# Kernel tuning notes

Hardware: AMD Instinct MI355X
Metric: run time of the kernel (lower is better)

The kernel has to match this reference:

```python
import jax, jax.numpy as jnp
import numpy as np

N_NODES = 100000
N_EDGES = 1600000
N_GRAPHS = 128
VOCAB = 10000
EMBED = 32
HID = 64
CLASSES = 2


def setup_inputs() -> dict:
    key = jax.random.key(0)
    ks = jax.random.split(key, 10)
    node_ids = jax.random.randint(ks[0], (N_NODES,), 0, VOCAB)
    edge_index = jax.random.randint(ks[1], (2, N_EDGES), 0, N_NODES)
    batch = jnp.sort(jax.random.randint(ks[2], (N_NODES,), 0, N_GRAPHS))
    s_e = 1.0 / np.sqrt(EMBED)
    s_h = 1.0 / np.sqrt(HID)
    return {
        "node_ids": node_ids,
        "edge_index": edge_index,
        "batch": batch,
        "embed_table": jax.random.normal(ks[3], (VOCAB, EMBED), jnp.float32),
        "W1_l": jax.random.normal(ks[4], (HID, EMBED), jnp.float32) * s_e,
        "W1_r": jax.random.normal(ks[5], (HID, EMBED), jnp.float32) * s_e,
        "b1": jnp.zeros((HID,), jnp.float32),
        "W2_l": jax.random.normal(ks[6], (HID, HID), jnp.float32) * s_h,
        "W2_r": jax.random.normal(ks[7], (HID, HID), jnp.float32) * s_h,
        "b2": jnp.zeros((HID,), jnp.float32),
        "W_lin": jax.random.normal(ks[8], (CLASSES, HID), jnp.float32) * s_h,
        "b_lin": jnp.zeros((CLASSES,), jnp.float32),
    }


def _sage_conv(x, src, dst, W_l, W_r, b):
    # mean-aggregate neighbor features: messages flow src -> dst
    msg_sum = jax.ops.segment_sum(x[src], dst, num_segments=x.shape[0])
    cnt = jax.ops.segment_sum(jnp.ones((src.shape[0], 1), x.dtype), dst,
                              num_segments=x.shape[0])
    mean = msg_sum / jnp.maximum(cnt, 1.0)
    return mean @ W_l.T + x @ W_r.T + b


def _global_mean_pool(x, batch, num_graphs):
    s = jax.ops.segment_sum(x, batch, num_segments=num_graphs)
    cnt = jax.ops.segment_sum(jnp.ones((x.shape[0], 1), x.dtype), batch,
                              num_segments=num_graphs)
    return s / jnp.maximum(cnt, 1.0)


def reference(node_ids, edge_index, batch, embed_table,
              W1_l, W1_r, b1, W2_l, W2_r, b2, W_lin, b_lin):
    src, dst = edge_index[0], edge_index[1]
    x = embed_table[node_ids]                       # [N, EMBED]
    x = jax.nn.relu(_sage_conv(x, src, dst, W1_l, W1_r, b1))  # [N, HID]
    x = jax.nn.relu(_sage_conv(x, src, dst, W2_l, W2_r, b2))  # [N, HID]
    g = _global_mean_pool(x, batch, N_GRAPHS)       # [G, HID]
    return g @ W_lin.T + b_lin                      # [G, CLASSES]
```

## Files before the change

### kernel.cpp

```cpp
#include <hip/hip_runtime.h>
#include <hip/hip_fp16.h>
#include <hip/hip_fp8.h>

#define N_NODES 100000
#define N_EDGES 1600000
#define N_GRAPHS 128
#define EMBED 32
#define HID 64
#define NBUCK 1563
#define CAP 1280
#define CHUNK 128
#define NGRP (N_EDGES / CHUNK)
#define PTILE 8192
#define NTILE ((N_EDGES + PTILE - 1) / PTILE)
#define TP 200
#define NPGRP 2048
#define PPER ((N_NODES + NPGRP - 1) / NPGRP)

typedef _Float16 f16x8 __attribute__((ext_vector_type(8)));
typedef float f32x4 __attribute__((ext_vector_type(4)));
typedef float f32x2 __attribute__((ext_vector_type(2)));
typedef unsigned short u16x8 __attribute__((ext_vector_type(8)));

__device__ __forceinline__ float fp8_to_f(unsigned char b) {
    __hip_fp8_e4m3 t; t.__x = (__hip_fp8_storage_t)b; return (float)t;
}
__device__ __forceinline__ unsigned char f_to_fp8(float f) {
    __hip_fp8_e4m3 t(f); return (unsigned char)t.__x;
}
__device__ __forceinline__ unsigned short h_bits(float f) {
    __half h = __float2half(f); return *(unsigned short*)&h;
}

#if defined(__has_builtin)
#if __has_builtin(__builtin_amdgcn_cvt_pk_f32_fp8)
#define HAVE_FP8_PK 1
#endif
#endif

__device__ __forceinline__ float2 fp8x2_to_f(unsigned short u) {
#ifdef HAVE_FP8_PK
    f32x2 r = __builtin_amdgcn_cvt_pk_f32_fp8((int)u, false);
    return make_float2(r[0], r[1]);
#else
    return make_float2(fp8_to_f((unsigned char)(u & 0xFF)),
                       fp8_to_f((unsigned char)(u >> 8)));
#endif
}

__global__ void k_embed(const int* __restrict__ ids,
                        const float* __restrict__ table,
                        __half2* __restrict__ x0h,
                        uchar2* __restrict__ x0q) {
    int gid = blockIdx.x * blockDim.x + threadIdx.x;
    int n = gid >> 4, q = gid & 15;
    int id = ids[n];
    float2 t = ((const float2*)(table + (size_t)id * EMBED))[q];
    x0h[(size_t)n * 16 + q] = __floats2half2_rn(t.x, t.y);
    x0q[(size_t)n * 16 + q] = make_uchar2(f_to_fp8(t.x), f_to_fp8(t.y));
}

__global__ __launch_bounds__(256)
void k_histA(const int* __restrict__ dst, int* __restrict__ bcnt,
             int* __restrict__ htile) {
    __shared__ int hist[NBUCK];
    int tid = threadIdx.x, t = blockIdx.x;
    int e0 = t * PTILE;
    int cnt = min(PTILE, N_EDGES - e0);
    for (int i = tid; i < NBUCK; i += 256) hist[i] = 0;
    __syncthreads();
    for (int i = tid; i < cnt; i += 256)
        atomicAdd(&hist[dst[e0 + i] >> 6], 1);
    __syncthreads();
    for (int b = tid; b < NBUCK; b += 256) {
        int v = hist[b];
        htile[b * TP + t] = v;
        if (v) atomicAdd(&bcnt[b], v);
    }
}

__global__ __launch_bounds__(1024)
void k_bscan(const int* __restrict__ bcnt, int* __restrict__ bbase,
             int* __restrict__ off_total) {
    __shared__ int leaf[1024];
    int t = threadIdx.x;
    int i0 = 2 * t, i1 = 2 * t + 1;
    int a = (i0 < NBUCK) ? bcnt[i0] : 0;
    int b = (i1 < NBUCK) ? bcnt[i1] : 0;
    leaf[t] = a + b;
    __syncthreads();
    for (int d = 1; d < 1024; d <<= 1) {
        int v = (t >= d) ? leaf[t - d] : 0;
        __syncthreads();
        leaf[t] += v;
        __syncthreads();
    }
    int excl = leaf[t] - (a + b);
    if (i0 < NBUCK) bbase[i0] = excl;
    if (i1 < NBUCK) bbase[i1] = excl + a;
    if (t == 1023) off_total[0] = leaf[1023];
}

__global__ __launch_bounds__(256)
void k_scanB(int* __restrict__ htile, const int* __restrict__ bbase) {
    int wv = threadIdx.x >> 6, lane = threadIdx.x & 63;
    int b = blockIdx.x * 4 + wv;
    if (b >= NBUCK) return;
    int* row = htile + b * TP;
    int v[4]; int s = 0;
    #pragma unroll
    for (int i = 0; i < 4; ++i) {
        int t = lane * 4 + i;
        v[i] = (t < NTILE) ? row[t] : 0;
        s += v[i];
    }
    int inc = s;
    for (int d = 1; d < 64; d <<= 1) {
        int u = __shfl_up(inc, d);
        if (lane >= d) inc += u;
    }
    int run = bbase[b] + inc - s;
    #pragma unroll
    for (int i = 0; i < 4; ++i) {
        int t = lane * 4 + i;
        if (t < NTILE) row[t] = run;
        run += v[i];
    }
}

__global__ __launch_bounds__(256)
void k_scatC(const int* __restrict__ src, const int* __restrict__ dst,
             const int* __restrict__ htile, int* __restrict__ epk) {
    __shared__ int cur[NBUCK];
    int orig = blockIdx.x;
    int xcd = orig & 7, idx = orig >> 3;
    const int q = NTILE >> 3, r = NTILE & 7;
    int t = (xcd < r ? xcd * (q + 1) : r * (q + 1) + (xcd - r) * q) + idx;
    int tid = threadIdx.x;
    int e0 = t * PTILE;
    int cnt = min(PTILE, N_EDGES - e0);
    for (int b = tid; b < NBUCK; b += 256) cur[b] = htile[b * TP + t];
    __syncthreads();
    for (int i = tid; i < cnt; i += 256) {
        int d = dst[e0 + i];
        int s = src[e0 + i];
        int b = d >> 6;
        int pos = atomicAdd(&cur[b], 1);
        epk[pos] = s | ((d & 63) << 17);
    }
}

__global__ __launch_bounds__(256)
void k_sortb(const int* __restrict__ bcnt, const int* __restrict__ epk,
             const int* __restrict__ bbase,
             int* __restrict__ ssrc, int* __restrict__ deg, int* __restrict__ off) {
    __shared__ int hist4[4][64];
    __shared__ int loff[64];
    __shared__ int cur4[4][64];
    int tid = threadIdx.x, bkt = blockIdx.x;
    int w = tid >> 6, lane = tid & 63;
    int base = bbase[bkt];
    int cntE = min(bcnt[bkt], CAP);
    hist4[w][lane] = 0;
    __syncthreads();
    const int* eb = epk + base;
    int v[5]; bool have[5];
    #pragma unroll
    for (int qq = 0; qq < 5; ++qq) {
        int i = qq * 256 + tid;
        have[qq] = (i < cntE);
        if (have[qq]) {
            v[qq] = eb[i];
            atomicAdd(&hist4[w][v[qq] >> 17], 1);
        }
    }
    __syncthreads();
    if (tid < 64) {
        int h0 = hist4[0][tid], h1 = hist4[1][tid];
        int h2 = hist4[2][tid], h3 = hist4[3][tid];
        int h = h0 + h1 + h2 + h3;
        int inc = h;
        for (int d = 1; d < 64; d <<= 1) {
            int u = __shfl_up(inc, d);
            if (tid >= d) inc += u;
        }
        int excl = inc - h;
        loff[tid] = excl;
        cur4[0][tid] = excl;
        cur4[1][tid] = excl + h0;
        cur4[2][tid] = excl + h0 + h1;
        cur4[3][tid] = excl + h0 + h1 + h2;
        int n0 = bkt << 6;
        if (n0 + tid < N_NODES) {
            deg[n0 + tid] = h;
            off[n0 + tid] = base + excl;
        }
    }
    __syncthreads();
    #pragma unroll
    for (int qq = 0; qq < 5; ++qq) {
        if (have[qq]) {
            int l = v[qq] >> 17;
            int pos = atomicAdd(&cur4[w][l], 1);
            ssrc[base + pos] = v[qq] & 0x1FFFF;
        }
    }
}

template<int L>
__global__ __launch_bounds__(256)
void k_agg(const int* __restrict__ ssrc, const int* __restrict__ off,
           const unsigned short* __restrict__ featq,
           float2* __restrict__ agg,
           float2* __restrict__ carry,
           int* __restrict__ carry_id)
{
    int tid = blockIdx.x * 256 + threadIdx.x;
    int grp = tid / L;
    int lane = tid % L;
    if (grp >= NGRP) return;
    int base = grp * CHUNK;
    int end  = base + CHUNK;
    int lo = 0, hi = N_NODES - 1;
    while (lo < hi) {
        int mid = (lo + hi + 1) >> 1;
        if (off[mid] <= base) lo = mid; else hi = mid - 1;
    }
    int d = lo;
    bool head = (off[d] >= base);
    int next = off[d + 1];
    float2 acc = make_float2(0.f, 0.f);
    for (int j = base; j < end; j += 8) {
        int4 pa = ((const int4*)(ssrc + j))[0];
        int4 pb = ((const int4*)(ssrc + j))[1];
        int ss[8] = {pa.x, pa.y, pa.z, pa.w, pb.x, pb.y, pb.z, pb.w};
        unsigned short v[8];
        #pragma unroll
        for (int q = 0; q < 8; ++q)
            v[q] = featq[(size_t)ss[q] * L + lane];
        #pragma unroll
        for (int q = 0; q < 8; ++q) {
            int jj = j + q;
            if (jj >= next) {
                if (head) {
                    agg[d * L + lane] = acc;
                } else {
                    carry[grp * L + lane] = acc;
                    if (lane == 0) carry_id[grp] = d;
                }
                acc = make_float2(0.f, 0.f);
                head = true;
                d++;
                while (off[d + 1] <= jj) d++;
                next = off[d + 1];
            }
            float2 f = fp8x2_to_f(v[q]);
            acc.x += f.x;
            acc.y += f.y;
        }
    }
    if (head) {
        agg[d * L + lane] = acc;
    } else {
        carry[grp * L + lane] = acc;
        if (lane == 0) carry_id[grp] = d;
    }
}

template<int L>
__global__ __launch_bounds__(256)
void k_fix(const float2* __restrict__ carry, const int* __restrict__ carry_id,
           float2* __restrict__ agg) {
    int tid = blockIdx.x * 256 + threadIdx.x;
    int grp = tid / L;
    int lane = tid % L;
    if (grp >= NGRP) return;
    int d = carry_id[grp];
    if (d < 0) return;
    float2 c = carry[grp * L + lane];
    unsafeAtomicAdd(&((float*)agg)[(d * L + lane) * 2],     c.x);
    unsafeAtomicAdd(&((float*)agg)[(d * L + lane) * 2 + 1], c.y);
}

template<int CIN, bool WQ8>
__global__ __launch_bounds__(256)
void k_updmm(const float* __restrict__ agg, const int* __restrict__ deg,
             const __half* __restrict__ own,
             const float* __restrict__ Wl, const float* __restrict__ Wr,
             const float* __restrict__ bias,
             __half* __restrict__ outh, unsigned char* __restrict__ outq) {
    constexpr int K = 2 * CIN;
    constexpr int C8 = K / 8;
    constexpr int ST = K + 8;
    __shared__ alignas(16) unsigned short catL[64 * ST];
    __shared__ alignas(16) unsigned short WLds[64 * ST];
    __shared__ float invL[64];
    int tid = threadIdx.x;
    int n0 = blockIdx.x * 64;
    int nn = min(64, N_NODES - n0);
    if (tid < 64) {
        int dg = (tid < nn) ? deg[n0 + tid] : 0;
        invL[tid] = (dg > 0) ? 1.0f / (float)dg : 0.0f;
    }
    for (int idx = tid; idx < 64 * C8; idx += 256) {
        int o = idx / C8, k = (idx % C8) * 8;
        const float* wsrc = (k < CIN) ? (Wl + o * CIN + k) : (Wr + o * CIN + k - CIN);
        float4 a = ((const float4*)wsrc)[0];
        float4 b = ((const float4*)wsrc)[1];
        u16x8 h = {h_bits(a.x), h_bits(a.y), h_bits(a.z), h_bits(a.w),
                   h_bits(b.x), h_bits(b.y), h_bits(b.z), h_bits(b.w)};
        *(u16x8*)&WLds[o * ST + k] = h;
    }
    __syncthreads();
    for (int idx = tid; idx < 64 * C8; idx += 256) {
        int n = idx / C8, k = (idx % C8) * 8;
        u16x8 h = {0, 0, 0, 0, 0, 0, 0, 0};
        if (n < nn) {
            if (k < CIN) {
                const float* as = agg + (size_t)(n0 + n) * CIN + k;
                float4 a = ((const float4*)as)[0];
                float4 b = ((const float4*)as)[1];
                float iv = invL[n];
                h = (u16x8){h_bits(a.x * iv), h_bits(a.y * iv),
                            h_bits(a.z * iv), h_bits(a.w * iv),
                            h_bits(b.x * iv), h_bits(b.y * iv),
                            h_bits(b.z * iv), h_bits(b.w * iv)};
            } else {
                h = *(const u16x8*)(own + (size_t)(n0 + n) * CIN + (k - CIN));
            }
        }
        *(u16x8*)&catL[n * ST + k] = h;
    }
    __syncthreads();
    int w = tid >> 6, lane = tid & 63;
    int nb = w * 16;
    if (nb >= nn) return;
    int col = lane & 15, g = lane >> 4;
    f16x8 aF[K / 32];
    #pragma unroll
    for (int ks = 0; ks < K / 32; ++ks)
        aF[ks] = *(const f16x8*)&catL[(nb + col) * ST + ks * 32 + g * 8];
    #pragma unroll
    for (int nt = 0; nt < 4; ++nt) {
        f32x4 c = {0.f, 0.f, 0.f, 0.f};
        #pragma unroll
        for (int ks = 0; ks < K / 32; ++ks) {
            f16x8 bF = *(const f16x8*)&WLds[(nt * 16 + col) * ST + ks * 32 + g * 8];
            c = __builtin_amdgcn_mfma_f32_16x16x32_f16(aF[ks], bF, c, 0, 0, 0);
        }
        int o = nt * 16 + col;
        float bo = bias[o];
        #pragma unroll
        for (int r = 0; r < 4; ++r) {
            int n = nb + g * 4 + r;
            if (n < nn) {
                float v = fmaxf(c[r] + bo, 0.f);
                outh[(size_t)(n0 + n) * HID + o] = __float2half(v);
                if constexpr (WQ8)
                    outq[(size_t)(n0 + n) * HID + o] = f_to_fp8(v);
            }
        }
    }
}

__global__ __launch_bounds__(256)
void k_pool_part(const __half* __restrict__ h2h, const int* __restrict__ batch,
                 float* __restrict__ pooled, float* __restrict__ gcnt) {
    int grp = blockIdx.x * 4 + (threadIdx.x >> 6);
    int lane = threadIdx.x & 63;
    int start = grp * PPER;
    if (start >= N_NODES) return;
    int end = start + PPER; if (end > N_NODES) end = N_NODES;
    float acc = 0.0f, c = 0.0f;
    int cur = batch[start];
    for (int n = start; n < end; ++n) {
        int bb = batch[n];
        if (bb != cur) {
            unsafeAtomicAdd(&pooled[cur * HID + lane], acc);
            if (lane == 0) unsafeAtomicAdd(&gcnt[cur], c);
            acc = 0.0f; c = 0.0f; cur = bb;
        }
        acc += __half2float(h2h[(size_t)n * HID + lane]);
        c += 1.0f;
    }
    unsafeAtomicAdd(&pooled[cur * HID + lane], acc);
    if (lane == 0) unsafeAtomicAdd(&gcnt[cur], c);
}

__global__ __launch_bounds__(256)
void k_final(const float* __restrict__ pooled, const float* __restrict__ gcnt,
             const float* __restrict__ W_lin, const float* __restrict__ b_lin,
             float* __restrict__ out) {
    int t = threadIdx.x;
    int g = t >> 1, c = t & 1;
    float inv = 1.0f / fmaxf(gcnt[g], 1.0f);
    float sum = b_lin[c];
    #pragma unroll 8
    for (int k = 0; k < HID; ++k)
        sum += pooled[g * HID + k] * inv * W_lin[c * HID + k];
    out[g * 2 + c] = sum;
}

extern "C" void kernel_launch(void* const* d_in, const int* in_sizes, int n_in,
                              void* d_out, int out_size, void* d_ws, size_t ws_size,
                              hipStream_t stream) {
    const int*   node_ids = (const int*)d_in[0];
    const int*   ei       = (const int*)d_in[1];
    const int*   batch    = (const int*)d_in[2];
    const float* table    = (const float*)d_in[3];
    const float* W1l      = (const float*)d_in[4];
    const float* W1r      = (const float*)d_in[5];
    const float* b1       = (const float*)d_in[6];
    const float* W2l      = (const float*)d_in[7];
    const float* W2r      = (const float*)d_in[8];
    const float* b2       = (const float*)d_in[9];
    const float* Wlin     = (const float*)d_in[10];
    const float* blin     = (const float*)d_in[11];
    const int* src = ei;
    const int* dst = ei + N_EDGES;

    int*   bcnt   = (int*)d_ws;
    float* pooled = (float*)(bcnt + 1600);
    float* gcnt   = pooled + 64 * N_GRAPHS;
    int* id16  = (int*)(gcnt + N_GRAPHS);
    int* id32  = id16 + NGRP;
    int* bbase = id32 + NGRP;
    int* ideg  = bbase + 1600;
    int* ioff  = ideg + N_NODES;
    int* htile = ioff + N_NODES + 1;
    int* epk   = htile + (size_t)NBUCK * TP;
    int* issrc = epk + N_EDGES;
    size_t int_total = 1600 + 8192 + 128 + NGRP + NGRP + 1600 + N_NODES
                     + (N_NODES + 1) + (size_t)NBUCK * TP + N_EDGES + N_EDGES;
    size_t falign = (int_total + 3) & ~(size_t)3;
    float*  aggAB = (float*)d_ws + falign;
    float2* c16   = (float2*)(aggAB + 64 * N_NODES);
    float2* c32   = (float2*)((float*)c16 + NGRP * 32);
    __half2* x0h  = (__half2*)((float*)c32 + NGRP * 64);
    __half*  h1h  = (__half*)(x0h + 16 * N_NODES);
    __half*  h2h  = h1h + 64 * N_NODES;
    uchar2*  x0q  = (uchar2*)(h2h + 64 * N_NODES);
    unsigned char* h1q = (unsigned char*)(x0q + 16 * N_NODES);

    hipMemsetAsync(bcnt, 0, (1600 + 8192 + 128) * sizeof(int), stream);
    hipMemsetAsync(id16, 0xFF, 2 * NGRP * sizeof(int), stream);

    k_embed<<<N_NODES * 16 / 256, 256, 0, stream>>>(node_ids, table, x0h, x0q);
    k_histA<<<NTILE, 256, 0, stream>>>(dst, bcnt, htile);
    k_bscan<<<1, 1024, 0, stream>>>(bcnt, bbase, ioff + N_NODES);
    k_scanB<<<(NBUCK + 3) / 4, 256, 0, stream>>>(htile, bbase);
    k_scatC<<<NTILE, 256, 0, stream>>>(src, dst, htile, epk);
    k_sortb<<<NBUCK, 256, 0, stream>>>(bcnt, epk, bbase, issrc, ideg, ioff);

    k_agg<16><<<(NGRP * 16 + 255) / 256, 256, 0, stream>>>(
        issrc, ioff, (const unsigned short*)x0q, (float2*)aggAB, c16, id16);
    k_fix<16><<<(NGRP * 16 + 255) / 256, 256, 0, stream>>>(c16, id16, (float2*)aggAB);
    k_updmm<EMBED, true><<<(N_NODES + 63) / 64, 256, 0, stream>>>(
        aggAB, ideg, (const __half*)x0h, W1l, W1r, b1, h1h, h1q);

    k_agg<32><<<(NGRP * 32 + 255) / 256, 256, 0, stream>>>(
        issrc, ioff, (const unsigned short*)h1q, (float2*)aggAB, c32, id32);
    k_fix<32><<<(NGRP * 32 + 255) / 256, 256, 0, stream>>>(c32, id32, (float2*)aggAB);
    k_updmm<HID, false><<<(N_NODES + 63) / 64, 256, 0, stream>>>(
        aggAB, ideg, h1h, W2l, W2r, b2, h2h, nullptr);

    k_pool_part<<<NPGRP / 4, 256, 0, stream>>>(h2h, batch, pooled, gcnt);
    k_final<<<1, 256, 0, stream>>>(pooled, gcnt, Wlin, blin, (float*)d_out);
}
```

Before: 208.9 us.

## Fuse embed, histogram and zero-init into one launch; reorder bucket scans

Merges the embedding gather, the per-tile destination histogram and the workspace zeroing into a single kernel, removing two memsets and one launch. The global atomic bucket counts are replaced by totals computed in the per-bucket tile scan, and the bucket base offset is added later in the scatter kernel, so the scans run in a different order. Layer 1 aggregation now gathers the fp16 embedding copy instead of an fp8 copy, which drops the fp8 write but doubles the gather bytes for that layer.

```diff
diff --git a/kernel.cpp b/kernel.cpp
--- a/kernel.cpp
+++ b/kernel.cpp
@@ -16,6 +16,7 @@
 #define TP 200
 #define NPGRP 2048
 #define PPER ((N_NODES + NPGRP - 1) / NPGRP)
+#define EMB_BLK (N_NODES * 16 / 256)
 
 typedef _Float16 f16x8 __attribute__((ext_vector_type(8)));
 typedef float f32x4 __attribute__((ext_vector_type(4)));
@@ -48,35 +49,65 @@
 #endif
 }
 
-__global__ void k_embed(const int* __restrict__ ids,
-                        const float* __restrict__ table,
-                        __half2* __restrict__ x0h,
-                        uchar2* __restrict__ x0q) {
-    int gid = blockIdx.x * blockDim.x + threadIdx.x;
-    int n = gid >> 4, q = gid & 15;
-    int id = ids[n];
-    float2 t = ((const float2*)(table + (size_t)id * EMBED))[q];
-    x0h[(size_t)n * 16 + q] = __floats2half2_rn(t.x, t.y);
-    x0q[(size_t)n * 16 + q] = make_uchar2(f_to_fp8(t.x), f_to_fp8(t.y));
-}
-
-__global__ __launch_bounds__(256)
-void k_histA(const int* __restrict__ dst, int* __restrict__ bcnt,
-             int* __restrict__ htile) {
+__global__ __launch_bounds__(256)
+void k_stage1(const int* __restrict__ ids, const float* __restrict__ table,
+              __half2* __restrict__ x0h,
+              const int* __restrict__ dst, int* __restrict__ htile,
+              float* __restrict__ zf, int* __restrict__ idf) {
     __shared__ int hist[NBUCK];
-    int tid = threadIdx.x, t = blockIdx.x;
-    int e0 = t * PTILE;
-    int cnt = min(PTILE, N_EDGES - e0);
-    for (int i = tid; i < NBUCK; i += 256) hist[i] = 0;
-    __syncthreads();
-    for (int i = tid; i < cnt; i += 256)
-        atomicAdd(&hist[dst[e0 + i] >> 6], 1);
-    __syncthreads();
-    for (int b = tid; b < NBUCK; b += 256) {
-        int v = hist[b];
-        htile[b * TP + t] = v;
-        if (v) atomicAdd(&bcnt[b], v);
-    }
+    int tid = threadIdx.x, b = blockIdx.x;
+    if (b < EMB_BLK) {
+        int gid = b * 256 + tid;
+        int n = gid >> 4, q = gid & 15;
+        int id = ids[n];
+        float2 t = ((const float2*)(table + (size_t)id * EMBED))[q];
+        x0h[(size_t)n * 16 + q] = __floats2half2_rn(t.x, t.y);
+        return;
+    }
+    if (b < EMB_BLK + NTILE) {
+        int t = b - EMB_BLK;
+        int e0 = t * PTILE;
+        int cnt = min(PTILE, N_EDGES - e0);
+        for (int i = tid; i < NBUCK; i += 256) hist[i] = 0;
+        __syncthreads();
+        for (int i = tid; i < cnt; i += 256)
+            atomicAdd(&hist[dst[e0 + i] >> 6], 1);
+        __syncthreads();
+        for (int bb = tid; bb < NBUCK; bb += 256)
+            htile[bb * TP + t] = hist[bb];
+        return;
+    }
+    for (int i = tid; i < 64 * N_GRAPHS + N_GRAPHS; i += 256) zf[i] = 0.f;
+    for (int i = tid; i < 2 * NGRP; i += 256) idf[i] = -1;
+}
+
+__global__ __launch_bounds__(256)
+void k_scanB(int* __restrict__ htile, int* __restrict__ bcnt) {
+    int wv = threadIdx.x >> 6, lane = threadIdx.x & 63;
+    int b = blockIdx.x * 4 + wv;
+    if (b >= NBUCK) return;
+    int* row = htile + b * TP;
+    int v[4]; int s = 0;
+    #pragma unroll
+    for (int i = 0; i < 4; ++i) {
+        int t = lane * 4 + i;
+        v[i] = (t < NTILE) ? row[t] : 0;
+        s += v[i];
+    }
+    int inc = s;
+    for (int d = 1; d < 64; d <<= 1) {
+        int u = __shfl_up(inc, d);
+        if (lane >= d) inc += u;
+    }
+    int run = inc - s;
+    #pragma unroll
+    for (int i = 0; i < 4; ++i) {
+        int t = lane * 4 + i;
+        if (t < NTILE) row[t] = run;
+        run += v[i];
+    }
+    int total = __shfl(inc, 63);
+    if (lane == 0) bcnt[b] = total;
 }
 
 __global__ __launch_bounds__(1024)
@@ -102,35 +133,9 @@
 }
 
 __global__ __launch_bounds__(256)
-void k_scanB(int* __restrict__ htile, const int* __restrict__ bbase) {
-    int wv = threadIdx.x >> 6, lane = threadIdx.x & 63;
-    int b = blockIdx.x * 4 + wv;
-    if (b >= NBUCK) return;
-    int* row = htile + b * TP;
-    int v[4]; int s = 0;
-    #pragma unroll
-    for (int i = 0; i < 4; ++i) {
-        int t = lane * 4 + i;
-        v[i] = (t < NTILE) ? row[t] : 0;
-        s += v[i];
-    }
-    int inc = s;
-    for (int d = 1; d < 64; d <<= 1) {
-        int u = __shfl_up(inc, d);
-        if (lane >= d) inc += u;
-    }
-    int run = bbase[b] + inc - s;
-    #pragma unroll
-    for (int i = 0; i < 4; ++i) {
-        int t = lane * 4 + i;
-        if (t < NTILE) row[t] = run;
-        run += v[i];
-    }
-}
-
-__global__ __launch_bounds__(256)
 void k_scatC(const int* __restrict__ src, const int* __restrict__ dst,
-             const int* __restrict__ htile, int* __restrict__ epk) {
+             const int* __restrict__ htile, const int* __restrict__ bbase,
+             int* __restrict__ epk) {
     __shared__ int cur[NBUCK];
     int orig = blockIdx.x;
     int xcd = orig & 7, idx = orig >> 3;
@@ -139,7 +144,8 @@
     int tid = threadIdx.x;
     int e0 = t * PTILE;
     int cnt = min(PTILE, N_EDGES - e0);
-    for (int b = tid; b < NBUCK; b += 256) cur[b] = htile[b * TP + t];
+    for (int b = tid; b < NBUCK; b += 256)
+        cur[b] = htile[b * TP + t] + bbase[b];
     __syncthreads();
     for (int i = tid; i < cnt; i += 256) {
         int d = dst[e0 + i];
@@ -207,14 +213,16 @@
     }
 }
 
-template<int L>
+template<int L, bool F16>
 __global__ __launch_bounds__(256)
 void k_agg(const int* __restrict__ ssrc, const int* __restrict__ off,
-           const unsigned short* __restrict__ featq,
+           const void* __restrict__ feat,
            float2* __restrict__ agg,
            float2* __restrict__ carry,
            int* __restrict__ carry_id)
 {
+    const unsigned int* f16p = (const unsigned int*)feat;
+    const unsigned short* f8p = (const unsigned short*)feat;
     int tid = blockIdx.x * 256 + threadIdx.x;
     int grp = tid / L;
     int lane = tid % L;
@@ -234,10 +242,12 @@
         int4 pa = ((const int4*)(ssrc + j))[0];
         int4 pb = ((const int4*)(ssrc + j))[1];
         int ss[8] = {pa.x, pa.y, pa.z, pa.w, pb.x, pb.y, pb.z, pb.w};
-        unsigned short v[8];
+        unsigned int v[8];
         #pragma unroll
-        for (int q = 0; q < 8; ++q)
-            v[q] = featq[(size_t)ss[q] * L + lane];
+        for (int q = 0; q < 8; ++q) {
+            size_t idx = (size_t)ss[q] * L + lane;
+            v[q] = F16 ? f16p[idx] : (unsigned int)f8p[idx];
+        }
         #pragma unroll
         for (int q = 0; q < 8; ++q) {
             int jj = j + q;
@@ -254,7 +264,13 @@
                 while (off[d + 1] <= jj) d++;
                 next = off[d + 1];
             }
-            float2 f = fp8x2_to_f(v[q]);
+            float2 f;
+            if constexpr (F16) {
+                __half2 h = *(__half2*)&v[q];
+                f = __half22float2(h);
+            } else {
+                f = fp8x2_to_f((unsigned short)v[q]);
+            }
             acc.x += f.x;
             acc.y += f.y;
         }
@@ -439,27 +455,23 @@
     __half2* x0h  = (__half2*)((float*)c32 + NGRP * 64);
     __half*  h1h  = (__half*)(x0h + 16 * N_NODES);
     __half*  h2h  = h1h + 64 * N_NODES;
-    uchar2*  x0q  = (uchar2*)(h2h + 64 * N_NODES);
-    unsigned char* h1q = (unsigned char*)(x0q + 16 * N_NODES);
-
-    hipMemsetAsync(bcnt, 0, (1600 + 8192 + 128) * sizeof(int), stream);
-    hipMemsetAsync(id16, 0xFF, 2 * NGRP * sizeof(int), stream);
-
-    k_embed<<<N_NODES * 16 / 256, 256, 0, stream>>>(node_ids, table, x0h, x0q);
-    k_histA<<<NTILE, 256, 0, stream>>>(dst, bcnt, htile);
+    unsigned char* h1q = (unsigned char*)(h2h + 64 * N_NODES);
+
+    k_stage1<<<EMB_BLK + NTILE + 1, 256, 0, stream>>>(node_ids, table, x0h,
+                                                      dst, htile, pooled, id16);
+    k_scanB<<<(NBUCK + 3) / 4, 256, 0, stream>>>(htile, bcnt);
     k_bscan<<<1, 1024, 0, stream>>>(bcnt, bbase, ioff + N_NODES);
-    k_scanB<<<(NBUCK + 3) / 4, 256, 0, stream>>>(htile, bbase);
-    k_scatC<<<NTILE, 256, 0, stream>>>(src, dst, htile, epk);
+    k_scatC<<<NTILE, 256, 0, stream>>>(src, dst, htile, bbase, epk);
     k_sortb<<<NBUCK, 256, 0, stream>>>(bcnt, epk, bbase, issrc, ideg, ioff);
 
-    k_agg<16><<<(NGRP * 16 + 255) / 256, 256, 0, stream>>>(
-        issrc, ioff, (const unsigned short*)x0q, (float2*)aggAB, c16, id16);
+    k_agg<16, true><<<(NGRP * 16 + 255) / 256, 256, 0, stream>>>(
+        issrc, ioff, (const void*)x0h, (float2*)aggAB, c16, id16);
     k_fix<16><<<(NGRP * 16 + 255) / 256, 256, 0, stream>>>(c16, id16, (float2*)aggAB);
     k_updmm<EMBED, true><<<(N_NODES + 63) / 64, 256, 0, stream>>>(
         aggAB, ideg, (const __half*)x0h, W1l, W1r, b1, h1h, h1q);
 
-    k_agg<32><<<(NGRP * 32 + 255) / 256, 256, 0, stream>>>(
-        issrc, ioff, (const unsigned short*)h1q, (float2*)aggAB, c32, id32);
+    k_agg<32, false><<<(NGRP * 32 + 255) / 256, 256, 0, stream>>>(
+        issrc, ioff, (const void*)h1q, (float2*)aggAB, c32, id32);
     k_fix<32><<<(NGRP * 32 + 255) / 256, 256, 0, stream>>>(c32, id32, (float2*)aggAB);
     k_updmm<HID, false><<<(N_NODES + 63) / 64, 256, 0, stream>>>(
         aggAB, ideg, h1h, W2l, W2r, b2, h2h, nullptr);
```

Result: no change. 205.2 us (-1.8%).
